# Kernel tuning notes

Measured on AMD Instinct MI355X. Metric: run time of the kernel, lower is better.

## Reference

```python
import jax, jax.numpy as jnp
import numpy as np

NUM_HEADS = 12
HEAD_SIZE = 64
HIDDEN = NUM_HEADS * HEAD_SIZE  # 768
SEQ = 4096


def setup_inputs() -> dict:
    key = jax.random.key(0)
    ks = jax.random.split(key, 7)
    s = 0.02
    return {
        "hidden_states": jax.random.normal(ks[0], (1, SEQ, HIDDEN), jnp.float32),
        "attention_mask": jnp.zeros((1, 1, 1, SEQ), jnp.float32),
        "Wq": jax.random.normal(ks[1], (HIDDEN, HIDDEN), jnp.float32) * s,
        "bq": jax.random.normal(ks[2], (HIDDEN,), jnp.float32) * s,
        "Wk": jax.random.normal(ks[3], (HIDDEN, HIDDEN), jnp.float32) * s,
        "bk": jax.random.normal(ks[4], (HIDDEN,), jnp.float32) * s,
        "Wv": jax.random.normal(ks[5], (HIDDEN, HIDDEN), jnp.float32) * s,
        "bv": jax.random.normal(ks[6], (HIDDEN,), jnp.float32) * s,
    }


def _split_heads(x):
    # [B, S, H] -> [B, nh, S, hd]
    B, S, _ = x.shape
    return x.reshape(B, S, NUM_HEADS, HEAD_SIZE).transpose(0, 2, 1, 3)


def reference(hidden_states, attention_mask, Wq, bq, Wk, bk, Wv, bv):
    # torch Linear: y = x @ W.T + b
    q = _split_heads(hidden_states @ Wq.T + bq)  # [B, nh, S, hd]
    k = _split_heads(hidden_states @ Wk.T + bk)
    scores = jnp.einsum("bhqd,bhkd->bhqk", q, k) / jnp.sqrt(
        jnp.asarray(HEAD_SIZE, hidden_states.dtype)
    )
    scores = scores + attention_mask  # broadcast [1,1,1,S]
    probs = jax.nn.softmax(scores, axis=-1)  # [B, nh, S, S]
    # multi_rand_attn_cuda is a Monte-Carlo approximation of the exact
    # aggregation: probs @ (hidden @ Wv.T + bv), per head. The reference
    # computes the exact expected value (deterministic equivalent).
    v = _split_heads(hidden_states @ Wv.T + bv)  # [B, nh, S, hd]
    ctx = jnp.einsum("bhqk,bhkd->bhqd", probs, v)  # [B, nh, S, hd]
    B, _, S, _ = ctx.shape
    ctx = ctx.transpose(0, 2, 1, 3).reshape(B, S, HIDDEN)
    return ctx
```

## Files before the change

kernel.cpp:

```cpp
#include <hip/hip_runtime.h>
#include <hip/hip_bf16.h>

#define SEQ 4096
#define HID 768
#define NHEAD 12
#define HDIM 64
#define KVB 64
#define NT (SEQ / KVB)
#define PBK 64
#define PNT (HID / PBK)

typedef __attribute__((ext_vector_type(8))) short bf16x8;
typedef __attribute__((ext_vector_type(4))) float f32x4;
typedef __attribute__((ext_vector_type(4))) short s16x4;

static __device__ __forceinline__ short f2bf(float f) {
    unsigned u = __builtin_bit_cast(unsigned, f);
    unsigned r = (u + 0x7fffu + ((u >> 16) & 1u)) >> 16;
    return (short)r;
}
static __device__ __forceinline__ unsigned cvtpk(float lo, float hi) {
    unsigned r;
    asm("v_cvt_pk_bf16_f32 %0, %1, %2" : "=v"(r) : "v"(lo), "v"(hi));
    return r;
}
static __device__ __forceinline__ float max3f(float a, float b, float c) {
    float r;
    asm("v_max3_f32 %0, %1, %2, %3" : "=v"(r) : "v"(a), "v"(b), "v"(c));
    return r;
}
static __device__ __forceinline__ void glds16(const void* g, void* l) {
    __builtin_amdgcn_global_load_lds(
        (const __attribute__((address_space(1))) unsigned*)g,
        (__attribute__((address_space(3))) unsigned*)l, 16, 0, 0);
}

__global__ __launch_bounds__(256) void cast_bf16_kernel(
    const float* __restrict__ src, short* __restrict__ dst)
{
    const size_t i = (size_t)blockIdx.x * 256 + threadIdx.x;
    const float4* s = reinterpret_cast<const float4*>(src) + i * 2;
    const float4 a = s[0], b = s[1];
    bf16x8 o;
    o[0] = f2bf(a.x); o[1] = f2bf(a.y); o[2] = f2bf(a.z); o[3] = f2bf(a.w);
    o[4] = f2bf(b.x); o[5] = f2bf(b.y); o[6] = f2bf(b.z); o[7] = f2bf(b.w);
    reinterpret_cast<bf16x8*>(dst)[i] = o;
}

__global__ __launch_bounds__(256) void cast_w_kernel(
    const float* __restrict__ Wq, const float* __restrict__ Wk,
    const float* __restrict__ Wv, short* __restrict__ dst)
{
    const int z = blockIdx.y;
    const float* src = (z == 0) ? Wq : ((z == 1) ? Wk : Wv);
    const size_t i = (size_t)blockIdx.x * 256 + threadIdx.x;
    const float4* s = reinterpret_cast<const float4*>(src) + i * 2;
    const float4 a = s[0], b = s[1];
    bf16x8 o;
    o[0] = f2bf(a.x); o[1] = f2bf(a.y); o[2] = f2bf(a.z); o[3] = f2bf(a.w);
    o[4] = f2bf(b.x); o[5] = f2bf(b.y); o[6] = f2bf(b.z); o[7] = f2bf(b.w);
    reinterpret_cast<bf16x8*>(dst + (size_t)z * HID * HID)[i] = o;
}

__global__ __launch_bounds__(256) void qkv_proj_kernel(
    const short* __restrict__ hsb, const short* __restrict__ Wb,
    const float* __restrict__ bq, const float* __restrict__ bk,
    const float* __restrict__ bv,
    short* __restrict__ Qb, short* __restrict__ Kb, short* __restrict__ Vt)
{
    __shared__ __align__(16) char lds[65536];
    const int z = blockIdx.z;
    const float* bias = (z == 0) ? bq : ((z == 1) ? bk : bv);

    const int lane = threadIdx.x & 63;
    const int w    = threadIdx.x >> 6;
    const int lr = lane & 15, hi = lane >> 4;
    const int wi = w >> 1, wj = w & 1;

    const short* Ag; const short* Bg; int ar0, br0;
    if (z < 2) { Ag = Wb + (size_t)z * HID * HID; ar0 = blockIdx.x * 128;
                 Bg = hsb;                        br0 = blockIdx.y * 128; }
    else       { Ag = hsb;                        ar0 = blockIdx.y * 128;
                 Bg = Wb + (size_t)2 * HID * HID; br0 = blockIdx.x * 128; }

    const int rsub = lane >> 3;
    const int c16  = (lane & 7) ^ rsub;

    auto stage = [&](int t, int buf) {
        const int k0 = t * PBK;
#pragma unroll
        for (int c = 0; c < 4; ++c) {
            const int ch = w * 4 + c;
            const int row = ch * 8 + rsub;
            glds16(Ag + (size_t)(ar0 + row) * HID + k0 + c16 * 8,
                   lds + buf * 16384 + ch * 1024);
            glds16(Bg + (size_t)(br0 + row) * HID + k0 + c16 * 8,
                   lds + 32768 + buf * 16384 + ch * 1024);
        }
    };

    stage(0, 0);
    f32x4 acc[4][4] = {};

    for (int t = 0; t < PNT; ++t) {
        asm volatile("s_waitcnt vmcnt(0)" ::: "memory");
        __builtin_amdgcn_s_barrier();
        __builtin_amdgcn_sched_barrier(0);
        if (t + 1 < PNT) stage(t + 1, (t + 1) & 1);
        const char* LA = lds + (t & 1) * 16384;
        const char* LB = lds + 32768 + (t & 1) * 16384;
#pragma unroll
        for (int ks = 0; ks < 2; ++ks) {
            bf16x8 af[4], bf_[4];
#pragma unroll
            for (int i = 0; i < 4; ++i) {
                const int rowA = wi * 64 + i * 16 + lr;
                af[i] = *reinterpret_cast<const bf16x8*>(
                    LA + rowA * 128 + (((ks * 4 + hi) ^ (rowA & 7)) << 4));
                const int rowB = wj * 64 + i * 16 + lr;
                bf_[i] = *reinterpret_cast<const bf16x8*>(
                    LB + rowB * 128 + (((ks * 4 + hi) ^ (rowB & 7)) << 4));
            }
            __builtin_amdgcn_s_setprio(1);
#pragma unroll
            for (int ia = 0; ia < 4; ++ia)
#pragma unroll
                for (int ib = 0; ib < 4; ++ib)
                    acc[ia][ib] = __builtin_amdgcn_mfma_f32_16x16x32_bf16(
                        af[ia], bf_[ib], acc[ia][ib], 0, 0, 0);
            __builtin_amdgcn_s_setprio(0);
        }
    }

    const float SCQ = 0.125f * 1.44269504088896340736f;
    if (z < 2) {
        short* outp = (z == 0) ? Qb : Kb;
        const float sc = (z == 0) ? SCQ : 1.0f;
#pragma unroll
        for (int ia = 0; ia < 4; ++ia) {
            const int nb = ar0 + wi * 64 + ia * 16 + hi * 4;
            const float4 b4 = *reinterpret_cast<const float4*>(bias + nb);
#pragma unroll
            for (int ib = 0; ib < 4; ++ib) {
                const int m = br0 + wj * 64 + ib * 16 + lr;
                s16x4 v;
                v[0] = f2bf((acc[ia][ib][0] + b4.x) * sc);
                v[1] = f2bf((acc[ia][ib][1] + b4.y) * sc);
                v[2] = f2bf((acc[ia][ib][2] + b4.z) * sc);
                v[3] = f2bf((acc[ia][ib][3] + b4.w) * sc);
                *reinterpret_cast<s16x4*>(outp + (size_t)m * HID + nb) = v;
            }
        }
    } else {
#pragma unroll
        for (int ib = 0; ib < 4; ++ib) {
            const int n = br0 + wj * 64 + ib * 16 + lr;
            const float bb = bias[n];
#pragma unroll
            for (int ia = 0; ia < 4; ++ia) {
                const int mb = ar0 + wi * 64 + ia * 16 + hi * 4;
                s16x4 v;
                v[0] = f2bf(acc[ia][ib][0] + bb);
                v[1] = f2bf(acc[ia][ib][1] + bb);
                v[2] = f2bf(acc[ia][ib][2] + bb);
                v[3] = f2bf(acc[ia][ib][3] + bb);
                *reinterpret_cast<s16x4*>(Vt + (size_t)n * SEQ + mb) = v;
            }
        }
    }
}

__global__ __launch_bounds__(256, 3) void attn_kernel(
    const short* __restrict__ Qb, const short* __restrict__ Kb,
    const short* __restrict__ Vt, const float* __restrict__ maskp,
    float* __restrict__ out)
{
    __shared__ __align__(16) char lds[49152];
    const int tid  = threadIdx.x;
    const int lane = tid & 63;
    const int w    = tid >> 6;
    const int lr = lane & 15, hi = lane >> 4;
    const int qh = w >> 1, kh = w & 1;
    const int h  = blockIdx.y;
    const int q0 = blockIdx.x * 64 + qh * 32;
    const float ML = 1.44269504088896340736f;

    const int srow = lane >> 3;
    int sofK[2], sofV[2];
    char* sdK[2][2]; char* sdV[2][2];
#pragma unroll
    for (int j = 0; j < 2; ++j) {
        const int ch  = w * 2 + j;
        const int row = ch * 8 + srow;
        const int c16 = (lane & 7) ^ srow ^ ((ch & 1) << 2);
        sofK[j] = row * HID + c16 * 8;
        sofV[j] = row * SEQ + c16 * 8;
#pragma unroll
        for (int b = 0; b < 2; ++b) {
            sdK[b][j] = lds + b * 8192 + ch * 1024;
            sdV[b][j] = lds + 16384 + b * 8192 + ch * 1024;
        }
    }
    const short* gK = Kb + h * HDIM;
    const short* gV = Vt + (size_t)h * HDIM * SEQ;

    auto stagep = [&](int buf) {
        glds16(gK + sofK[0], sdK[buf][0]);
        glds16(gK + sofK[1], sdK[buf][1]);
        glds16(gV + sofV[0], sdV[buf][0]);
        glds16(gV + sofV[1], sdV[buf][1]);
        gK += KVB * HID; gV += KVB;
    };

    stagep(0);

    {
        float* mb = (float*)(lds + 32768);
        const int base = tid * 16;
#pragma unroll
        for (int i = 0; i < 4; ++i) {
            float4 m4 = *reinterpret_cast<const float4*>(maskp + base + i * 4);
            m4.x *= ML; m4.y *= ML; m4.z *= ML; m4.w *= ML;
            *reinterpret_cast<float4*>(mb + base + i * 4) = m4;
        }
    }

    const short* qp = Qb + (size_t)(q0 + lr) * HID + h * HDIM + hi * 8;
    const bf16x8 qf0 = *reinterpret_cast<const bf16x8*>(qp);
    const bf16x8 qf1 = *reinterpret_cast<const bf16x8*>(qp + 32);
    bf16x8 qg0, qg1;
    {
        const short* qp2 = qp + 16 * HID;
        qg0 = *reinterpret_cast<const bf16x8*>(qp2);
        qg1 = *reinterpret_cast<const bf16x8*>(qp2 + 32);
    }

    const int kbase = ((lr >> 2) * 8) + (lr & 3) + kh * 32;
    const int fv    = (lr & 7) ^ (((lr >> 3) & 1) << 2);
    const int vslot = ((kh * 4 + hi) ^ fv) << 4;
    const char* kp[2][2][2];
    const char* vp[2][4];
#pragma unroll
    for (int b = 0; b < 2; ++b) {
#pragma unroll
        for (int kg = 0; kg < 2; ++kg) {
            const int row = kbase + kg * 4;
            const int fr  = (row & 7) ^ ((row >> 1) & 4);
            kp[b][kg][0] = lds + b * 8192 + row * 128 + ((hi ^ fr) << 4);
            kp[b][kg][1] = lds + b * 8192 + row * 128 + (((4 + hi) ^ fr) << 4);
        }
#pragma unroll
        for (int dg = 0; dg < 4; ++dg)
            vp[b][dg] = lds + 16384 + b * 8192 + (dg * 16 + lr) * 128 + vslot;
    }
    const float* mptr = (const float*)(lds + 32768) + kh * 32 + hi * 8;

    __syncthreads();

    f32x4 acc[4][2] = {};
    float m_r[2] = {-INFINITY, -INFINITY};
    float ls[2]  = {0.f, 0.f};

    auto tile = [&](int tt, int buf) {
        asm volatile("s_waitcnt vmcnt(0)" ::: "memory");
        __builtin_amdgcn_s_barrier();
        __builtin_amdgcn_sched_barrier(0);
        if (tt + 1 < NT) stagep(buf ^ 1);

        const f32x4 ci0 = *reinterpret_cast<const f32x4*>(mptr);
        const f32x4 ci1 = *reinterpret_cast<const f32x4*>(mptr + 4);
        mptr += KVB;
        const bf16x8 kf00 = *reinterpret_cast<const bf16x8*>(kp[buf][0][0]);
        const bf16x8 kf01 = *reinterpret_cast<const bf16x8*>(kp[buf][0][1]);
        const bf16x8 kf10 = *reinterpret_cast<const bf16x8*>(kp[buf][1][0]);
        const bf16x8 kf11 = *reinterpret_cast<const bf16x8*>(kp[buf][1][1]);
        f32x4 z[2][2];
        z[0][0] = ci0; z[0][1] = ci0; z[1][0] = ci1; z[1][1] = ci1;
        __builtin_amdgcn_s_setprio(1);
        z[0][0] = __builtin_amdgcn_mfma_f32_16x16x32_bf16(kf00, qf0, z[0][0], 0, 0, 0);
        z[0][0] = __builtin_amdgcn_mfma_f32_16x16x32_bf16(kf01, qf1, z[0][0], 0, 0, 0);
        z[0][1] = __builtin_amdgcn_mfma_f32_16x16x32_bf16(kf00, qg0, z[0][1], 0, 0, 0);
        z[0][1] = __builtin_amdgcn_mfma_f32_16x16x32_bf16(kf01, qg1, z[0][1], 0, 0, 0);
        z[1][0] = __builtin_amdgcn_mfma_f32_16x16x32_bf16(kf10, qf0, z[1][0], 0, 0, 0);
        z[1][0] = __builtin_amdgcn_mfma_f32_16x16x32_bf16(kf11, qf1, z[1][0], 0, 0, 0);
        z[1][1] = __builtin_amdgcn_mfma_f32_16x16x32_bf16(kf10, qg0, z[1][1], 0, 0, 0);
        z[1][1] = __builtin_amdgcn_mfma_f32_16x16x32_bf16(kf11, qg1, z[1][1], 0, 0, 0);
        __builtin_amdgcn_s_setprio(0);

        float e_[2][2][4];
#pragma unroll
        for (int kg = 0; kg < 2; ++kg)
#pragma unroll
            for (int qg = 0; qg < 2; ++qg)
#pragma unroll
                for (int r = 0; r < 4; ++r)
                    e_[kg][qg][r] = exp2f(z[kg][qg][r] - m_r[qg]);

        const float pa = max3f(e_[0][0][0], e_[0][0][1], e_[0][0][2]);
        const float pb = max3f(e_[0][0][3], e_[0][1][0], e_[0][1][1]);
        const float pc = max3f(e_[0][1][2], e_[0][1][3], e_[1][0][0]);
        const float pd = max3f(e_[1][0][1], e_[1][0][2], e_[1][0][3]);
        const float pe = max3f(e_[1][1][0], e_[1][1][1], e_[1][1][2]);
        const float pmax = max3f(fmaxf(pa, pb), fmaxf(pc, pd),
                                 fmaxf(pe, e_[1][1][3]));
        if (__ballot(pmax > 256.f)) {
#pragma unroll
            for (int qg = 0; qg < 2; ++qg) {
                float t_ = fmaxf(
                    max3f(z[0][qg][0], z[0][qg][1], z[0][qg][2]),
                    max3f(fmaxf(z[0][qg][3], z[1][qg][0]),
                          fmaxf(z[1][qg][1], z[1][qg][2]), z[1][qg][3]));
                t_ = fmaxf(t_, __shfl_xor(t_, 16));
                t_ = fmaxf(t_, __shfl_xor(t_, 32));
                const float newm = fmaxf(m_r[qg], t_);
                const float sc = exp2f(fmaxf(m_r[qg] - newm, -128.f));
                ls[qg] *= sc;
#pragma unroll
                for (int dg = 0; dg < 4; ++dg) acc[dg][qg] *= sc;
                m_r[qg] = newm;
#pragma unroll
                for (int kg = 0; kg < 2; ++kg)
#pragma unroll
                    for (int r = 0; r < 4; ++r)
                        e_[kg][qg][r] = exp2f(z[kg][qg][r] - newm);
            }
        }

        union { unsigned u[4]; bf16x8 v; } P[2];
#pragma unroll
        for (int qg = 0; qg < 2; ++qg) {
            ls[qg] += ((e_[0][qg][0] + e_[0][qg][1]) + (e_[0][qg][2] + e_[0][qg][3]))
                    + ((e_[1][qg][0] + e_[1][qg][1]) + (e_[1][qg][2] + e_[1][qg][3]));
            P[qg].u[0] = cvtpk(e_[0][qg][0], e_[0][qg][1]);
            P[qg].u[1] = cvtpk(e_[0][qg][2], e_[0][qg][3]);
            P[qg].u[2] = cvtpk(e_[1][qg][0], e_[1][qg][1]);
            P[qg].u[3] = cvtpk(e_[1][qg][2], e_[1][qg][3]);
        }

#pragma unroll
        for (int dg = 0; dg < 4; ++dg) {
            const bf16x8 vf = *reinterpret_cast<const bf16x8*>(vp[buf][dg]);
            __builtin_amdgcn_s_setprio(1);
            acc[dg][0] = __builtin_amdgcn_mfma_f32_16x16x32_bf16(vf, P[0].v, acc[dg][0], 0, 0, 0);
            acc[dg][1] = __builtin_amdgcn_mfma_f32_16x16x32_bf16(vf, P[1].v, acc[dg][1], 0, 0, 0);
            __builtin_amdgcn_s_setprio(0);
        }
    };

    for (int t = 0; t < NT; t += 2) {
        tile(t, 0);
        tile(t + 1, 1);
    }

#pragma unroll
    for (int qg = 0; qg < 2; ++qg) {
        float t_ = ls[qg];
        t_ += __shfl_xor(t_, 16);
        t_ += __shfl_xor(t_, 32);
        ls[qg] = t_;
    }

    __syncthreads();
    float* mg  = (float*)lds;
    float* mlb = (float*)(lds + 16384);
    if (kh == 1) {
#pragma unroll
        for (int qg = 0; qg < 2; ++qg) {
            float2 v0; v0.x = m_r[qg]; v0.y = ls[qg];
            *reinterpret_cast<float2*>(mlb + (((qh * 2 + qg) * 64 + lane) * 2)) = v0;
        }
#pragma unroll
        for (int dg = 0; dg < 4; ++dg)
#pragma unroll
            for (int qg = 0; qg < 2; ++qg)
                *reinterpret_cast<f32x4*>(
                    mg + ((qh * 8 + dg * 2 + qg) * 64 + lane) * 4) = acc[dg][qg];
    }
    __syncthreads();
    if (kh == 0) {
        float sc0[2], sc1[2], rl[2];
#pragma unroll
        for (int qg = 0; qg < 2; ++qg) {
            const float2 v = *reinterpret_cast<const float2*>(
                mlb + (((qh * 2 + qg) * 64 + lane) * 2));
            const float mm = fmaxf(m_r[qg], v.x);
            sc0[qg] = exp2f(fmaxf(m_r[qg] - mm, -128.f));
            sc1[qg] = exp2f(fmaxf(v.x - mm, -128.f));
            rl[qg] = 1.0f / (ls[qg] * sc0[qg] + v.y * sc1[qg]);
        }
#pragma unroll
        for (int dg = 0; dg < 4; ++dg) {
#pragma unroll
            for (int qg = 0; qg < 2; ++qg) {
                const f32x4 o1 = *reinterpret_cast<const f32x4*>(
                    mg + ((qh * 8 + dg * 2 + qg) * 64 + lane) * 4);
                const f32x4 of = (acc[dg][qg] * sc0[qg] + o1 * sc1[qg]) * rl[qg];
                float* op = out + (size_t)(q0 + qg * 16 + lr) * HID
                          + h * HDIM + dg * 16 + hi * 4;
                *reinterpret_cast<f32x4*>(op) = of;
            }
        }
    }
}

extern "C" void kernel_launch(void* const* d_in, const int* in_sizes, int n_in,
                              void* d_out, int out_size, void* d_ws, size_t ws_size,
                              hipStream_t stream) {
    const float* hs   = (const float*)d_in[0];
    const float* mask = (const float*)d_in[1];
    const float* Wq   = (const float*)d_in[2];
    const float* bq   = (const float*)d_in[3];
    const float* Wk   = (const float*)d_in[4];
    const float* bk   = (const float*)d_in[5];
    const float* Wv   = (const float*)d_in[6];
    const float* bv   = (const float*)d_in[7];

    short* Qb = (short*)d_ws;
    short* Kb = Qb + (size_t)SEQ * HID;
    short* Vt = Kb + (size_t)SEQ * HID;
    float* out = (float*)d_out;

    short* hsb = (short*)d_out;
    short* Wb  = hsb + (size_t)SEQ * HID;

    cast_bf16_kernel<<<dim3(SEQ * HID / 2048), 256, 0, stream>>>(hs, hsb);
    cast_w_kernel<<<dim3(HID * HID / 2048, 3), 256, 0, stream>>>(Wq, Wk, Wv, Wb);

    qkv_proj_kernel<<<dim3(HID / 128, SEQ / 128, 3), 256, 0, stream>>>(
        hsb, Wb, bq, bk, bv, Qb, Kb, Vt);

    attn_kernel<<<dim3(SEQ / KVB, NHEAD), 256, 0, stream>>>(Qb, Kb, Vt, mask, out);
}
```

Measured before the change: 130.6 us.

## Load K/V tiles directly into registers with prefetch instead of LDS staging

The attention kernel no longer stages K and V tiles through double-buffered LDS with barriers. Each wave now loads its own MFMA fragments for K, V and the mask straight from global memory into registers, prefetching the next tile one iteration ahead. The mask scaling by log2(e) moves into a separate small kernel that writes to workspace. This removes per-tile barriers and LDS traffic and cuts LDS use to the final merge buffer. In exchange it duplicates global/L2 loads across the waves that share a key tile, uses strided, less coalesced accesses, and raises register pressure under the 3-block launch bound.

```diff
diff --git a/kernel.cpp b/kernel.cpp
--- a/kernel.cpp
+++ b/kernel.cpp
@@ -62,6 +62,16 @@
     reinterpret_cast<bf16x8*>(dst + (size_t)z * HID * HID)[i] = o;
 }
 
+__global__ __launch_bounds__(256) void maskml_kernel(
+    const float* __restrict__ m, float* __restrict__ o)
+{
+    const float ML = 1.44269504088896340736f;
+    const int i = blockIdx.x * 256 + threadIdx.x;
+    float4 v = reinterpret_cast<const float4*>(m)[i];
+    v.x *= ML; v.y *= ML; v.z *= ML; v.w *= ML;
+    reinterpret_cast<float4*>(o)[i] = v;
+}
+
 __global__ __launch_bounds__(256) void qkv_proj_kernel(
     const short* __restrict__ hsb, const short* __restrict__ Wb,
     const float* __restrict__ bq, const float* __restrict__ bk,
@@ -172,10 +182,10 @@
 
 __global__ __launch_bounds__(256, 3) void attn_kernel(
     const short* __restrict__ Qb, const short* __restrict__ Kb,
-    const short* __restrict__ Vt, const float* __restrict__ maskp,
+    const short* __restrict__ Vt, const float* __restrict__ maskml,
     float* __restrict__ out)
 {
-    __shared__ __align__(16) char lds[49152];
+    __shared__ __align__(16) char lds[18432];
     const int tid  = threadIdx.x;
     const int lane = tid & 63;
     const int w    = tid >> 6;
@@ -183,108 +193,68 @@
     const int qh = w >> 1, kh = w & 1;
     const int h  = blockIdx.y;
     const int q0 = blockIdx.x * 64 + qh * 32;
-    const float ML = 1.44269504088896340736f;
-
-    const int srow = lane >> 3;
-    int sofK[2], sofV[2];
-    char* sdK[2][2]; char* sdV[2][2];
-#pragma unroll
-    for (int j = 0; j < 2; ++j) {
-        const int ch  = w * 2 + j;
-        const int row = ch * 8 + srow;
-        const int c16 = (lane & 7) ^ srow ^ ((ch & 1) << 2);
-        sofK[j] = row * HID + c16 * 8;
-        sofV[j] = row * SEQ + c16 * 8;
-#pragma unroll
-        for (int b = 0; b < 2; ++b) {
-            sdK[b][j] = lds + b * 8192 + ch * 1024;
-            sdV[b][j] = lds + 16384 + b * 8192 + ch * 1024;
-        }
-    }
-    const short* gK = Kb + h * HDIM;
-    const short* gV = Vt + (size_t)h * HDIM * SEQ;
-
-    auto stagep = [&](int buf) {
-        glds16(gK + sofK[0], sdK[buf][0]);
-        glds16(gK + sofK[1], sdK[buf][1]);
-        glds16(gV + sofV[0], sdV[buf][0]);
-        glds16(gV + sofV[1], sdV[buf][1]);
-        gK += KVB * HID; gV += KVB;
+
+    const int kbase = ((lr >> 2) * 8) + (lr & 3) + kh * 32;
+    const int oK0 = kbase * HID + h * HDIM + hi * 8;
+    const int oK1 = oK0 + 32;
+    const int oK2 = (kbase + 4) * HID + h * HDIM + hi * 8;
+    const int oK3 = oK2 + 32;
+    int oV[4];
+#pragma unroll
+    for (int dg = 0; dg < 4; ++dg)
+        oV[dg] = (h * HDIM + dg * 16 + lr) * SEQ + kh * 32 + hi * 8;
+    const int oM = kh * 32 + hi * 8;
+
+    struct KV {
+        bf16x8 k00, k01, k10, k11;
+        bf16x8 v0, v1, v2, v3;
+        f32x4 ci0, ci1;
     };
-
-    stagep(0);
-
-    {
-        float* mb = (float*)(lds + 32768);
-        const int base = tid * 16;
-#pragma unroll
-        for (int i = 0; i < 4; ++i) {
-            float4 m4 = *reinterpret_cast<const float4*>(maskp + base + i * 4);
-            m4.x *= ML; m4.y *= ML; m4.z *= ML; m4.w *= ML;
-            *reinterpret_cast<float4*>(mb + base + i * 4) = m4;
-        }
-    }
+    auto loadKV = [&](int t) {
+        KV f;
+        const short* k = Kb + (size_t)t * KVB * HID;
+        f.k00 = *reinterpret_cast<const bf16x8*>(k + oK0);
+        f.k01 = *reinterpret_cast<const bf16x8*>(k + oK1);
+        f.k10 = *reinterpret_cast<const bf16x8*>(k + oK2);
+        f.k11 = *reinterpret_cast<const bf16x8*>(k + oK3);
+        const short* v = Vt + t * KVB;
+        f.v0 = *reinterpret_cast<const bf16x8*>(v + oV[0]);
+        f.v1 = *reinterpret_cast<const bf16x8*>(v + oV[1]);
+        f.v2 = *reinterpret_cast<const bf16x8*>(v + oV[2]);
+        f.v3 = *reinterpret_cast<const bf16x8*>(v + oV[3]);
+        const float* m = maskml + t * KVB;
+        f.ci0 = *reinterpret_cast<const f32x4*>(m + oM);
+        f.ci1 = *reinterpret_cast<const f32x4*>(m + oM + 4);
+        return f;
+    };
 
     const short* qp = Qb + (size_t)(q0 + lr) * HID + h * HDIM + hi * 8;
     const bf16x8 qf0 = *reinterpret_cast<const bf16x8*>(qp);
     const bf16x8 qf1 = *reinterpret_cast<const bf16x8*>(qp + 32);
-    bf16x8 qg0, qg1;
-    {
-        const short* qp2 = qp + 16 * HID;
-        qg0 = *reinterpret_cast<const bf16x8*>(qp2);
-        qg1 = *reinterpret_cast<const bf16x8*>(qp2 + 32);
-    }
-
-    const int kbase = ((lr >> 2) * 8) + (lr & 3) + kh * 32;
-    const int fv    = (lr & 7) ^ (((lr >> 3) & 1) << 2);
-    const int vslot = ((kh * 4 + hi) ^ fv) << 4;
-    const char* kp[2][2][2];
-    const char* vp[2][4];
-#pragma unroll
-    for (int b = 0; b < 2; ++b) {
-#pragma unroll
-        for (int kg = 0; kg < 2; ++kg) {
-            const int row = kbase + kg * 4;
-            const int fr  = (row & 7) ^ ((row >> 1) & 4);
-            kp[b][kg][0] = lds + b * 8192 + row * 128 + ((hi ^ fr) << 4);
-            kp[b][kg][1] = lds + b * 8192 + row * 128 + (((4 + hi) ^ fr) << 4);
-        }
-#pragma unroll
-        for (int dg = 0; dg < 4; ++dg)
-            vp[b][dg] = lds + 16384 + b * 8192 + (dg * 16 + lr) * 128 + vslot;
-    }
-    const float* mptr = (const float*)(lds + 32768) + kh * 32 + hi * 8;
-
-    __syncthreads();
+    const bf16x8 qg0 = *reinterpret_cast<const bf16x8*>(qp + 16 * HID);
+    const bf16x8 qg1 = *reinterpret_cast<const bf16x8*>(qp + 16 * HID + 32);
 
     f32x4 acc[4][2] = {};
     float m_r[2] = {-INFINITY, -INFINITY};
     float ls[2]  = {0.f, 0.f};
 
-    auto tile = [&](int tt, int buf) {
-        asm volatile("s_waitcnt vmcnt(0)" ::: "memory");
-        __builtin_amdgcn_s_barrier();
-        __builtin_amdgcn_sched_barrier(0);
-        if (tt + 1 < NT) stagep(buf ^ 1);
-
-        const f32x4 ci0 = *reinterpret_cast<const f32x4*>(mptr);
-        const f32x4 ci1 = *reinterpret_cast<const f32x4*>(mptr + 4);
-        mptr += KVB;
-        const bf16x8 kf00 = *reinterpret_cast<const bf16x8*>(kp[buf][0][0]);
-        const bf16x8 kf01 = *reinterpret_cast<const bf16x8*>(kp[buf][0][1]);
-        const bf16x8 kf10 = *reinterpret_cast<const bf16x8*>(kp[buf][1][0]);
-        const bf16x8 kf11 = *reinterpret_cast<const bf16x8*>(kp[buf][1][1]);
+    KV cur = loadKV(0);
+
+    for (int t = 0; t < NT; ++t) {
+        KV nxt = loadKV((t + 1) & (NT - 1));
+
         f32x4 z[2][2];
-        z[0][0] = ci0; z[0][1] = ci0; z[1][0] = ci1; z[1][1] = ci1;
+        z[0][0] = cur.ci0; z[0][1] = cur.ci0;
+        z[1][0] = cur.ci1; z[1][1] = cur.ci1;
         __builtin_amdgcn_s_setprio(1);
-        z[0][0] = __builtin_amdgcn_mfma_f32_16x16x32_bf16(kf00, qf0, z[0][0], 0, 0, 0);
-        z[0][0] = __builtin_amdgcn_mfma_f32_16x16x32_bf16(kf01, qf1, z[0][0], 0, 0, 0);
-        z[0][1] = __builtin_amdgcn_mfma_f32_16x16x32_bf16(kf00, qg0, z[0][1], 0, 0, 0);
-        z[0][1] = __builtin_amdgcn_mfma_f32_16x16x32_bf16(kf01, qg1, z[0][1], 0, 0, 0);
-        z[1][0] = __builtin_amdgcn_mfma_f32_16x16x32_bf16(kf10, qf0, z[1][0], 0, 0, 0);
-        z[1][0] = __builtin_amdgcn_mfma_f32_16x16x32_bf16(kf11, qf1, z[1][0], 0, 0, 0);
-        z[1][1] = __builtin_amdgcn_mfma_f32_16x16x32_bf16(kf10, qg0, z[1][1], 0, 0, 0);
-        z[1][1] = __builtin_amdgcn_mfma_f32_16x16x32_bf16(kf11, qg1, z[1][1], 0, 0, 0);
+        z[0][0] = __builtin_amdgcn_mfma_f32_16x16x32_bf16(cur.k00, qf0, z[0][0], 0, 0, 0);
+        z[0][0] = __builtin_amdgcn_mfma_f32_16x16x32_bf16(cur.k01, qf1, z[0][0], 0, 0, 0);
+        z[0][1] = __builtin_amdgcn_mfma_f32_16x16x32_bf16(cur.k00, qg0, z[0][1], 0, 0, 0);
+        z[0][1] = __builtin_amdgcn_mfma_f32_16x16x32_bf16(cur.k01, qg1, z[0][1], 0, 0, 0);
+        z[1][0] = __builtin_amdgcn_mfma_f32_16x16x32_bf16(cur.k10, qf0, z[1][0], 0, 0, 0);
+        z[1][0] = __builtin_amdgcn_mfma_f32_16x16x32_bf16(cur.k11, qf1, z[1][0], 0, 0, 0);
+        z[1][1] = __builtin_amdgcn_mfma_f32_16x16x32_bf16(cur.k10, qg0, z[1][1], 0, 0, 0);
+        z[1][1] = __builtin_amdgcn_mfma_f32_16x16x32_bf16(cur.k11, qg1, z[1][1], 0, 0, 0);
         __builtin_amdgcn_s_setprio(0);
 
         float e_[2][2][4];
@@ -337,19 +307,18 @@
             P[qg].u[3] = cvtpk(e_[1][qg][2], e_[1][qg][3]);
         }
 
-#pragma unroll
-        for (int dg = 0; dg < 4; ++dg) {
-            const bf16x8 vf = *reinterpret_cast<const bf16x8*>(vp[buf][dg]);
-            __builtin_amdgcn_s_setprio(1);
-            acc[dg][0] = __builtin_amdgcn_mfma_f32_16x16x32_bf16(vf, P[0].v, acc[dg][0], 0, 0, 0);
-            acc[dg][1] = __builtin_amdgcn_mfma_f32_16x16x32_bf16(vf, P[1].v, acc[dg][1], 0, 0, 0);
-            __builtin_amdgcn_s_setprio(0);
-        }
-    };
-
-    for (int t = 0; t < NT; t += 2) {
-        tile(t, 0);
-        tile(t + 1, 1);
+        __builtin_amdgcn_s_setprio(1);
+        acc[0][0] = __builtin_amdgcn_mfma_f32_16x16x32_bf16(cur.v0, P[0].v, acc[0][0], 0, 0, 0);
+        acc[0][1] = __builtin_amdgcn_mfma_f32_16x16x32_bf16(cur.v0, P[1].v, acc[0][1], 0, 0, 0);
+        acc[1][0] = __builtin_amdgcn_mfma_f32_16x16x32_bf16(cur.v1, P[0].v, acc[1][0], 0, 0, 0);
+        acc[1][1] = __builtin_amdgcn_mfma_f32_16x16x32_bf16(cur.v1, P[1].v, acc[1][1], 0, 0, 0);
+        acc[2][0] = __builtin_amdgcn_mfma_f32_16x16x32_bf16(cur.v2, P[0].v, acc[2][0], 0, 0, 0);
+        acc[2][1] = __builtin_amdgcn_mfma_f32_16x16x32_bf16(cur.v2, P[1].v, acc[2][1], 0, 0, 0);
+        acc[3][0] = __builtin_amdgcn_mfma_f32_16x16x32_bf16(cur.v3, P[0].v, acc[3][0], 0, 0, 0);
+        acc[3][1] = __builtin_amdgcn_mfma_f32_16x16x32_bf16(cur.v3, P[1].v, acc[3][1], 0, 0, 0);
+        __builtin_amdgcn_s_setprio(0);
+
+        cur = nxt;
     }
 
 #pragma unroll
@@ -360,7 +329,6 @@
         ls[qg] = t_;
     }
 
-    __syncthreads();
     float* mg  = (float*)lds;
     float* mlb = (float*)(lds + 16384);
     if (kh == 1) {
@@ -418,6 +386,7 @@
     short* Qb = (short*)d_ws;
     short* Kb = Qb + (size_t)SEQ * HID;
     short* Vt = Kb + (size_t)SEQ * HID;
+    float* maskML = (float*)(Vt + (size_t)HID * SEQ);
     float* out = (float*)d_out;
 
     short* hsb = (short*)d_out;
@@ -425,9 +394,10 @@
 
     cast_bf16_kernel<<<dim3(SEQ * HID / 2048), 256, 0, stream>>>(hs, hsb);
     cast_w_kernel<<<dim3(HID * HID / 2048, 3), 256, 0, stream>>>(Wq, Wk, Wv, Wb);
+    maskml_kernel<<<dim3(SEQ / 1024), 256, 0, stream>>>(mask, maskML);
 
     qkv_proj_kernel<<<dim3(HID / 128, SEQ / 128, 3), 256, 0, stream>>>(
         hsb, Wb, bq, bk, bv, Qb, Kb, Vt);
 
-    attn_kernel<<<dim3(SEQ / KVB, NHEAD), 256, 0, stream>>>(Qb, Kb, Vt, mask, out);
-}
+    attn_kernel<<<dim3(SEQ / KVB, NHEAD), 256, 0, stream>>>(Qb, Kb, Vt, maskML, out);
+}
```

Measured after the change: 228.6 us. +75.1%, slower.

## Triple-buffer K/V staging in attention and precompute scaled mask in separate kernel

Applied to the files above, without the earlier changes.

Changes the attention kernel's K/V LDS staging from double to triple buffering with prefetch distance two, waiting on vmcnt(6) instead of draining all loads each tile. The log2e-scaled mask moves out of LDS into a small pre-kernel, and each tile loads the next tile's mask values from global into registers. This is meant to hide more global load latency and drop the per-block mask LDS fill, at the cost of more LDS (48KB used for K/V), an extra kernel launch, and per-tile global mask loads. The final iterations issue wrapped-around redundant prefetches.

```diff
diff --git a/kernel.cpp b/kernel.cpp
--- a/kernel.cpp
+++ b/kernel.cpp
@@ -62,6 +62,16 @@
     reinterpret_cast<bf16x8*>(dst + (size_t)z * HID * HID)[i] = o;
 }
 
+__global__ __launch_bounds__(256) void maskml_kernel(
+    const float* __restrict__ m, float* __restrict__ o)
+{
+    const float ML = 1.44269504088896340736f;
+    const int i = blockIdx.x * 256 + threadIdx.x;
+    float4 v = reinterpret_cast<const float4*>(m)[i];
+    v.x *= ML; v.y *= ML; v.z *= ML; v.w *= ML;
+    reinterpret_cast<float4*>(o)[i] = v;
+}
+
 __global__ __launch_bounds__(256) void qkv_proj_kernel(
     const short* __restrict__ hsb, const short* __restrict__ Wb,
     const float* __restrict__ bq, const float* __restrict__ bk,
@@ -172,7 +182,7 @@
 
 __global__ __launch_bounds__(256, 3) void attn_kernel(
     const short* __restrict__ Qb, const short* __restrict__ Kb,
-    const short* __restrict__ Vt, const float* __restrict__ maskp,
+    const short* __restrict__ Vt, const float* __restrict__ maskml,
     float* __restrict__ out)
 {
     __shared__ __align__(16) char lds[49152];
@@ -183,65 +193,57 @@
     const int qh = w >> 1, kh = w & 1;
     const int h  = blockIdx.y;
     const int q0 = blockIdx.x * 64 + qh * 32;
-    const float ML = 1.44269504088896340736f;
 
     const int srow = lane >> 3;
     int sofK[2], sofV[2];
-    char* sdK[2][2]; char* sdV[2][2];
+    char* sdK_[3][2]; char* sdV_[3][2];
 #pragma unroll
     for (int j = 0; j < 2; ++j) {
         const int ch  = w * 2 + j;
         const int row = ch * 8 + srow;
         const int c16 = (lane & 7) ^ srow ^ ((ch & 1) << 2);
-        sofK[j] = row * HID + c16 * 8;
-        sofV[j] = row * SEQ + c16 * 8;
-#pragma unroll
-        for (int b = 0; b < 2; ++b) {
-            sdK[b][j] = lds + b * 8192 + ch * 1024;
-            sdV[b][j] = lds + 16384 + b * 8192 + ch * 1024;
-        }
-    }
-    const short* gK = Kb + h * HDIM;
-    const short* gV = Vt + (size_t)h * HDIM * SEQ;
-
-    auto stagep = [&](int buf) {
-        glds16(gK + sofK[0], sdK[buf][0]);
-        glds16(gK + sofK[1], sdK[buf][1]);
-        glds16(gV + sofV[0], sdV[buf][0]);
-        glds16(gV + sofV[1], sdV[buf][1]);
-        gK += KVB * HID; gV += KVB;
+        sofK[j] = row * HID + h * HDIM + c16 * 8;
+        sofV[j] = (h * HDIM + row) * SEQ + c16 * 8;
+#pragma unroll
+        for (int b = 0; b < 3; ++b) {
+            sdK_[b][j] = lds + b * 8192 + ch * 1024;
+            sdV_[b][j] = lds + 24576 + b * 8192 + ch * 1024;
+        }
+    }
+
+    auto stagep = [&](int slot, int tn) {
+        const short* k = Kb + (size_t)tn * (KVB * HID);
+        const short* v = Vt + tn * KVB;
+        glds16(k + sofK[0], sdK_[slot][0]);
+        glds16(k + sofK[1], sdK_[slot][1]);
+        glds16(v + sofV[0], sdV_[slot][0]);
+        glds16(v + sofV[1], sdV_[slot][1]);
     };
-
-    stagep(0);
-
-    {
-        float* mb = (float*)(lds + 32768);
-        const int base = tid * 16;
-#pragma unroll
-        for (int i = 0; i < 4; ++i) {
-            float4 m4 = *reinterpret_cast<const float4*>(maskp + base + i * 4);
-            m4.x *= ML; m4.y *= ML; m4.z *= ML; m4.w *= ML;
-            *reinterpret_cast<float4*>(mb + base + i * 4) = m4;
-        }
-    }
+    const int oM = kh * 32 + hi * 8;
+    auto loadM = [&](int tn, f32x4& a, f32x4& b) {
+        const float* m = maskml + tn * KVB + oM;
+        a = *reinterpret_cast<const f32x4*>(m);
+        b = *reinterpret_cast<const f32x4*>(m + 4);
+    };
 
     const short* qp = Qb + (size_t)(q0 + lr) * HID + h * HDIM + hi * 8;
     const bf16x8 qf0 = *reinterpret_cast<const bf16x8*>(qp);
     const bf16x8 qf1 = *reinterpret_cast<const bf16x8*>(qp + 32);
-    bf16x8 qg0, qg1;
-    {
-        const short* qp2 = qp + 16 * HID;
-        qg0 = *reinterpret_cast<const bf16x8*>(qp2);
-        qg1 = *reinterpret_cast<const bf16x8*>(qp2 + 32);
-    }
+    const bf16x8 qg0 = *reinterpret_cast<const bf16x8*>(qp + 16 * HID);
+    const bf16x8 qg1 = *reinterpret_cast<const bf16x8*>(qp + 16 * HID + 32);
+
+    f32x4 cm0, cm1;
+    stagep(0, 0);
+    loadM(0, cm0, cm1);
+    stagep(1, 1);
 
     const int kbase = ((lr >> 2) * 8) + (lr & 3) + kh * 32;
     const int fv    = (lr & 7) ^ (((lr >> 3) & 1) << 2);
     const int vslot = ((kh * 4 + hi) ^ fv) << 4;
-    const char* kp[2][2][2];
-    const char* vp[2][4];
-#pragma unroll
-    for (int b = 0; b < 2; ++b) {
+    const char* kp[3][2][2];
+    const char* vp[3][4];
+#pragma unroll
+    for (int b = 0; b < 3; ++b) {
 #pragma unroll
         for (int kg = 0; kg < 2; ++kg) {
             const int row = kbase + kg * 4;
@@ -251,31 +253,29 @@
         }
 #pragma unroll
         for (int dg = 0; dg < 4; ++dg)
-            vp[b][dg] = lds + 16384 + b * 8192 + (dg * 16 + lr) * 128 + vslot;
-    }
-    const float* mptr = (const float*)(lds + 32768) + kh * 32 + hi * 8;
-
-    __syncthreads();
+            vp[b][dg] = lds + 24576 + b * 8192 + (dg * 16 + lr) * 128 + vslot;
+    }
 
     f32x4 acc[4][2] = {};
     float m_r[2] = {-INFINITY, -INFINITY};
     float ls[2]  = {0.f, 0.f};
 
-    auto tile = [&](int tt, int buf) {
-        asm volatile("s_waitcnt vmcnt(0)" ::: "memory");
+    auto tile = [&](int tt, const int rs, const int ws) {
+        asm volatile("s_waitcnt vmcnt(6)" ::: "memory");
         __builtin_amdgcn_s_barrier();
         __builtin_amdgcn_sched_barrier(0);
-        if (tt + 1 < NT) stagep(buf ^ 1);
-
-        const f32x4 ci0 = *reinterpret_cast<const f32x4*>(mptr);
-        const f32x4 ci1 = *reinterpret_cast<const f32x4*>(mptr + 4);
-        mptr += KVB;
-        const bf16x8 kf00 = *reinterpret_cast<const bf16x8*>(kp[buf][0][0]);
-        const bf16x8 kf01 = *reinterpret_cast<const bf16x8*>(kp[buf][0][1]);
-        const bf16x8 kf10 = *reinterpret_cast<const bf16x8*>(kp[buf][1][0]);
-        const bf16x8 kf11 = *reinterpret_cast<const bf16x8*>(kp[buf][1][1]);
+        f32x4 nm0, nm1;
+        loadM((tt + 1) & (NT - 1), nm0, nm1);
+        __builtin_amdgcn_sched_barrier(0);
+        stagep(ws, (tt + 2) & (NT - 1));
+        __builtin_amdgcn_sched_barrier(0);
+
+        const bf16x8 kf00 = *reinterpret_cast<const bf16x8*>(kp[rs][0][0]);
+        const bf16x8 kf01 = *reinterpret_cast<const bf16x8*>(kp[rs][0][1]);
+        const bf16x8 kf10 = *reinterpret_cast<const bf16x8*>(kp[rs][1][0]);
+        const bf16x8 kf11 = *reinterpret_cast<const bf16x8*>(kp[rs][1][1]);
         f32x4 z[2][2];
-        z[0][0] = ci0; z[0][1] = ci0; z[1][0] = ci1; z[1][1] = ci1;
+        z[0][0] = cm0; z[0][1] = cm0; z[1][0] = cm1; z[1][1] = cm1;
         __builtin_amdgcn_s_setprio(1);
         z[0][0] = __builtin_amdgcn_mfma_f32_16x16x32_bf16(kf00, qf0, z[0][0], 0, 0, 0);
         z[0][0] = __builtin_amdgcn_mfma_f32_16x16x32_bf16(kf01, qf1, z[0][0], 0, 0, 0);
@@ -339,18 +339,23 @@
 
 #pragma unroll
         for (int dg = 0; dg < 4; ++dg) {
-            const bf16x8 vf = *reinterpret_cast<const bf16x8*>(vp[buf][dg]);
+            const bf16x8 vf = *reinterpret_cast<const bf16x8*>(vp[rs][dg]);
             __builtin_amdgcn_s_setprio(1);
             acc[dg][0] = __builtin_amdgcn_mfma_f32_16x16x32_bf16(vf, P[0].v, acc[dg][0], 0, 0, 0);
             acc[dg][1] = __builtin_amdgcn_mfma_f32_16x16x32_bf16(vf, P[1].v, acc[dg][1], 0, 0, 0);
             __builtin_amdgcn_s_setprio(0);
         }
+        cm0 = nm0; cm1 = nm1;
     };
 
-    for (int t = 0; t < NT; t += 2) {
-        tile(t, 0);
-        tile(t + 1, 1);
-    }
+    int t = 0;
+#pragma unroll 1
+    for (int i = 0; i < 21; ++i) {
+        tile(t, 0, 2); ++t;
+        tile(t, 1, 0); ++t;
+        tile(t, 2, 1); ++t;
+    }
+    tile(63, 0, 2);
 
 #pragma unroll
     for (int qg = 0; qg < 2; ++qg) {
@@ -418,6 +423,7 @@
     short* Qb = (short*)d_ws;
     short* Kb = Qb + (size_t)SEQ * HID;
     short* Vt = Kb + (size_t)SEQ * HID;
+    float* maskML = (float*)(Vt + (size_t)HID * SEQ);
     float* out = (float*)d_out;
 
     short* hsb = (short*)d_out;
@@ -425,9 +431,10 @@
 
     cast_bf16_kernel<<<dim3(SEQ * HID / 2048), 256, 0, stream>>>(hs, hsb);
     cast_w_kernel<<<dim3(HID * HID / 2048, 3), 256, 0, stream>>>(Wq, Wk, Wv, Wb);
+    maskml_kernel<<<dim3(SEQ / 1024), 256, 0, stream>>>(mask, maskML);
 
     qkv_proj_kernel<<<dim3(HID / 128, SEQ / 128, 3), 256, 0, stream>>>(
         hsb, Wb, bq, bk, bv, Qb, Kb, Vt);
 
-    attn_kernel<<<dim3(SEQ / KVB, NHEAD), 256, 0, stream>>>(Qb, Kb, Vt, mask, out);
-}
+    attn_kernel<<<dim3(SEQ / KVB, NHEAD), 256, 0, stream>>>(Qb, Kb, Vt, maskML, out);
+}
```

Measured after the change: 139.3 us. 6.7% more time.

## Shrink attention blocks to two waves with private KV buffers and no barriers

Applied to the files above, without the earlier changes.

The attention kernel drops from 4 waves and 64 queries per block to 2 waves and 32 queries per block. Each wave stages its own half of the K/V tile into a private LDS double buffer, so the per-tile block barrier goes away. The mask pre-scale by log2(e) moves into a separate tiny kernel, and the mask is read from global memory each tile. Blocks are swizzled over (head, q-tile) and the grid doubles, which trades more blocks and redundant Q loads for less synchronisation and better XCD/L2 locality.

```diff
diff --git a/kernel.cpp b/kernel.cpp
--- a/kernel.cpp
+++ b/kernel.cpp
@@ -62,6 +62,16 @@
     reinterpret_cast<bf16x8*>(dst + (size_t)z * HID * HID)[i] = o;
 }
 
+__global__ __launch_bounds__(256) void maskml_kernel(
+    const float* __restrict__ m, float* __restrict__ o)
+{
+    const float ML = 1.44269504088896340736f;
+    const int i = blockIdx.x * 256 + threadIdx.x;
+    float4 v = reinterpret_cast<const float4*>(m)[i];
+    v.x *= ML; v.y *= ML; v.z *= ML; v.w *= ML;
+    reinterpret_cast<float4*>(o)[i] = v;
+}
+
 __global__ __launch_bounds__(256) void qkv_proj_kernel(
     const short* __restrict__ hsb, const short* __restrict__ Wb,
     const float* __restrict__ bq, const float* __restrict__ bk,
@@ -170,92 +180,69 @@
     }
 }
 
-__global__ __launch_bounds__(256, 3) void attn_kernel(
+__global__ __launch_bounds__(128, 2) void attn_kernel(
     const short* __restrict__ Qb, const short* __restrict__ Kb,
-    const short* __restrict__ Vt, const float* __restrict__ maskp,
+    const short* __restrict__ Vt, const float* __restrict__ maskml,
     float* __restrict__ out)
 {
-    __shared__ __align__(16) char lds[49152];
+    __shared__ __align__(16) char lds[32768];
     const int tid  = threadIdx.x;
     const int lane = tid & 63;
-    const int w    = tid >> 6;
+    const int kh   = tid >> 6;
     const int lr = lane & 15, hi = lane >> 4;
-    const int qh = w >> 1, kh = w & 1;
-    const int h  = blockIdx.y;
-    const int q0 = blockIdx.x * 64 + qh * 32;
-    const float ML = 1.44269504088896340736f;
+
+    const int bid = blockIdx.x;
+    const int swz = (bid & 7) * 192 + (bid >> 3);
+    const int head = swz >> 7;
+    const int q0   = (swz & 127) * 32;
+
+    char* wbuf = lds + kh * 16384;
 
     const int srow = lane >> 3;
-    int sofK[2], sofV[2];
-    char* sdK[2][2]; char* sdV[2][2];
-#pragma unroll
-    for (int j = 0; j < 2; ++j) {
-        const int ch  = w * 2 + j;
-        const int row = ch * 8 + srow;
-        const int c16 = (lane & 7) ^ srow ^ ((ch & 1) << 2);
-        sofK[j] = row * HID + c16 * 8;
-        sofV[j] = row * SEQ + c16 * 8;
-#pragma unroll
-        for (int b = 0; b < 2; ++b) {
-            sdK[b][j] = lds + b * 8192 + ch * 1024;
-            sdV[b][j] = lds + 16384 + b * 8192 + ch * 1024;
-        }
-    }
-    const short* gK = Kb + h * HDIM;
-    const short* gV = Vt + (size_t)h * HDIM * SEQ;
-
-    auto stagep = [&](int buf) {
-        glds16(gK + sofK[0], sdK[buf][0]);
-        glds16(gK + sofK[1], sdK[buf][1]);
-        glds16(gV + sofV[0], sdV[buf][0]);
-        glds16(gV + sofV[1], sdV[buf][1]);
-        gK += KVB * HID; gV += KVB;
+    size_t sofK[4]; size_t sofV[4];
+#pragma unroll
+    for (int j = 0; j < 4; ++j) {
+        const int c16 = (lane & 7) ^ srow ^ ((j & 1) << 2);
+        sofK[j] = (size_t)(kh * 32 + j * 8 + srow) * HID + head * HDIM + c16 * 8;
+        sofV[j] = (size_t)(head * HDIM + j * 16 + (lane >> 2)) * SEQ
+                + kh * 32 + (lane & 3) * 8;
+    }
+    auto stagep = [&](int buf, int tn) {
+        const short* kb = Kb + (size_t)tn * (KVB * HID);
+        const short* vb = Vt + tn * KVB;
+        char* d = wbuf + buf * 8192;
+#pragma unroll
+        for (int j = 0; j < 4; ++j) glds16(kb + sofK[j], d + j * 1024);
+#pragma unroll
+        for (int j = 0; j < 4; ++j) glds16(vb + sofV[j], d + 4096 + j * 1024);
     };
 
-    stagep(0);
-
-    {
-        float* mb = (float*)(lds + 32768);
-        const int base = tid * 16;
-#pragma unroll
-        for (int i = 0; i < 4; ++i) {
-            float4 m4 = *reinterpret_cast<const float4*>(maskp + base + i * 4);
-            m4.x *= ML; m4.y *= ML; m4.z *= ML; m4.w *= ML;
-            *reinterpret_cast<float4*>(mb + base + i * 4) = m4;
-        }
-    }
-
-    const short* qp = Qb + (size_t)(q0 + lr) * HID + h * HDIM + hi * 8;
+    const short* qp = Qb + (size_t)(q0 + lr) * HID + head * HDIM + hi * 8;
     const bf16x8 qf0 = *reinterpret_cast<const bf16x8*>(qp);
     const bf16x8 qf1 = *reinterpret_cast<const bf16x8*>(qp + 32);
-    bf16x8 qg0, qg1;
-    {
-        const short* qp2 = qp + 16 * HID;
-        qg0 = *reinterpret_cast<const bf16x8*>(qp2);
-        qg1 = *reinterpret_cast<const bf16x8*>(qp2 + 32);
-    }
-
-    const int kbase = ((lr >> 2) * 8) + (lr & 3) + kh * 32;
-    const int fv    = (lr & 7) ^ (((lr >> 3) & 1) << 2);
-    const int vslot = ((kh * 4 + hi) ^ fv) << 4;
+    const bf16x8 qg0 = *reinterpret_cast<const bf16x8*>(qp + 16 * HID);
+    const bf16x8 qg1 = *reinterpret_cast<const bf16x8*>(qp + 16 * HID + 32);
+
+    stagep(0, 0);
+    asm volatile("s_waitcnt vmcnt(0)" ::: "memory");
+
+    const int kbl = ((lr >> 2) * 8) + (lr & 3);
     const char* kp[2][2][2];
     const char* vp[2][4];
 #pragma unroll
     for (int b = 0; b < 2; ++b) {
 #pragma unroll
         for (int kg = 0; kg < 2; ++kg) {
-            const int row = kbase + kg * 4;
-            const int fr  = (row & 7) ^ ((row >> 1) & 4);
-            kp[b][kg][0] = lds + b * 8192 + row * 128 + ((hi ^ fr) << 4);
-            kp[b][kg][1] = lds + b * 8192 + row * 128 + (((4 + hi) ^ fr) << 4);
+            const int row = kbl + kg * 4;
+            const int fr  = (row & 7) ^ (((row >> 3) & 1) << 2);
+            kp[b][kg][0] = wbuf + b * 8192 + row * 128 + ((hi ^ fr) << 4);
+            kp[b][kg][1] = wbuf + b * 8192 + row * 128 + (((4 + hi) ^ fr) << 4);
         }
 #pragma unroll
         for (int dg = 0; dg < 4; ++dg)
-            vp[b][dg] = lds + 16384 + b * 8192 + (dg * 16 + lr) * 128 + vslot;
-    }
-    const float* mptr = (const float*)(lds + 32768) + kh * 32 + hi * 8;
-
-    __syncthreads();
+            vp[b][dg] = wbuf + b * 8192 + 4096 + (dg * 16 + lr) * 64 + (hi << 4);
+    }
+    const float* mbase = maskml + kh * 32 + hi * 8;
 
     f32x4 acc[4][2] = {};
     float m_r[2] = {-INFINITY, -INFINITY};
@@ -263,13 +250,12 @@
 
     auto tile = [&](int tt, int buf) {
         asm volatile("s_waitcnt vmcnt(0)" ::: "memory");
-        __builtin_amdgcn_s_barrier();
         __builtin_amdgcn_sched_barrier(0);
-        if (tt + 1 < NT) stagep(buf ^ 1);
-
-        const f32x4 ci0 = *reinterpret_cast<const f32x4*>(mptr);
-        const f32x4 ci1 = *reinterpret_cast<const f32x4*>(mptr + 4);
-        mptr += KVB;
+        stagep(buf ^ 1, (tt + 1) & (NT - 1));
+        const float* mp = mbase + tt * KVB;
+        const f32x4 ci0 = *reinterpret_cast<const f32x4*>(mp);
+        const f32x4 ci1 = *reinterpret_cast<const f32x4*>(mp + 4);
+
         const bf16x8 kf00 = *reinterpret_cast<const bf16x8*>(kp[buf][0][0]);
         const bf16x8 kf01 = *reinterpret_cast<const bf16x8*>(kp[buf][0][1]);
         const bf16x8 kf10 = *reinterpret_cast<const bf16x8*>(kp[buf][1][0]);
@@ -347,6 +333,7 @@
         }
     };
 
+#pragma unroll 1
     for (int t = 0; t < NT; t += 2) {
         tile(t, 0);
         tile(t + 1, 1);
@@ -362,19 +349,19 @@
 
     __syncthreads();
     float* mg  = (float*)lds;
-    float* mlb = (float*)(lds + 16384);
+    float* mlb = (float*)(lds + 8192);
     if (kh == 1) {
 #pragma unroll
         for (int qg = 0; qg < 2; ++qg) {
             float2 v0; v0.x = m_r[qg]; v0.y = ls[qg];
-            *reinterpret_cast<float2*>(mlb + (((qh * 2 + qg) * 64 + lane) * 2)) = v0;
+            *reinterpret_cast<float2*>(mlb + ((qg * 64 + lane) * 2)) = v0;
         }
 #pragma unroll
         for (int dg = 0; dg < 4; ++dg)
 #pragma unroll
             for (int qg = 0; qg < 2; ++qg)
                 *reinterpret_cast<f32x4*>(
-                    mg + ((qh * 8 + dg * 2 + qg) * 64 + lane) * 4) = acc[dg][qg];
+                    mg + ((dg * 2 + qg) * 64 + lane) * 4) = acc[dg][qg];
     }
     __syncthreads();
     if (kh == 0) {
@@ -382,7 +369,7 @@
 #pragma unroll
         for (int qg = 0; qg < 2; ++qg) {
             const float2 v = *reinterpret_cast<const float2*>(
-                mlb + (((qh * 2 + qg) * 64 + lane) * 2));
+                mlb + ((qg * 64 + lane) * 2));
             const float mm = fmaxf(m_r[qg], v.x);
             sc0[qg] = exp2f(fmaxf(m_r[qg] - mm, -128.f));
             sc1[qg] = exp2f(fmaxf(v.x - mm, -128.f));
@@ -393,10 +380,10 @@
 #pragma unroll
             for (int qg = 0; qg < 2; ++qg) {
                 const f32x4 o1 = *reinterpret_cast<const f32x4*>(
-                    mg + ((qh * 8 + dg * 2 + qg) * 64 + lane) * 4);
+                    mg + ((dg * 2 + qg) * 64 + lane) * 4);
                 const f32x4 of = (acc[dg][qg] * sc0[qg] + o1 * sc1[qg]) * rl[qg];
                 float* op = out + (size_t)(q0 + qg * 16 + lr) * HID
-                          + h * HDIM + dg * 16 + hi * 4;
+                          + head * HDIM + dg * 16 + hi * 4;
                 *reinterpret_cast<f32x4*>(op) = of;
             }
         }
@@ -418,6 +405,7 @@
     short* Qb = (short*)d_ws;
     short* Kb = Qb + (size_t)SEQ * HID;
     short* Vt = Kb + (size_t)SEQ * HID;
+    float* maskML = (float*)(Vt + (size_t)HID * SEQ);
     float* out = (float*)d_out;
 
     short* hsb = (short*)d_out;
@@ -425,9 +413,10 @@
 
     cast_bf16_kernel<<<dim3(SEQ * HID / 2048), 256, 0, stream>>>(hs, hsb);
     cast_w_kernel<<<dim3(HID * HID / 2048, 3), 256, 0, stream>>>(Wq, Wk, Wv, Wb);
+    maskml_kernel<<<dim3(SEQ / 1024), 256, 0, stream>>>(mask, maskML);
 
     qkv_proj_kernel<<<dim3(HID / 128, SEQ / 128, 3), 256, 0, stream>>>(
         hsb, Wb, bq, bk, bv, Qb, Kb, Vt);
 
-    attn_kernel<<<dim3(SEQ / KVB, NHEAD), 256, 0, stream>>>(Qb, Kb, Vt, mask, out);
-}
+    attn_kernel<<<dim3(SEQ * NHEAD / 32), 128, 0, stream>>>(Qb, Kb, Vt, maskML, out);
+}
```

Result: slower. 206.4 us (+58.1%).
